# Kernel tuning notes

Measured on AMD Instinct MI355X. Metric: run time of the kernel, lower is better.

The kernel has to match this reference:

```python
import jax, jax.numpy as jnp
import numpy as np

T, B, IN, HID, OUT = 256, 64, 1024, 1024, 1024


def setup_inputs() -> dict:
    key = jax.random.key(0)
    ks = jax.random.split(key, 16)
    w = lambda k, i, o: (0.01 * jax.random.normal(k, (i, o), dtype=jnp.float32))
    return {
        "steps": jax.random.normal(ks[0], (T, B, IN), dtype=jnp.float32),
        "h": jax.random.normal(ks[1], (B, HID), dtype=jnp.float32),
        "c": jax.random.normal(ks[2], (B, HID), dtype=jnp.float32),
        "Wfx": w(ks[3], IN, HID), "Wfh": w(ks[4], HID, HID), "bf": jnp.zeros(HID, jnp.float32),
        "Wix": w(ks[5], IN, HID), "Wih": w(ks[6], HID, HID), "bi": jnp.zeros(HID, jnp.float32),
        "Wcx": w(ks[7], IN, HID), "Wch": w(ks[8], HID, HID), "bc": jnp.zeros(HID, jnp.float32),
        "Wox": w(ks[9], IN, HID), "Woh": w(ks[10], HID, HID), "bo": jnp.zeros(HID, jnp.float32),
        "Wy": w(ks[11], HID, OUT), "by": jnp.zeros(OUT, jnp.float32),
    }


def reference(steps, h, c, Wfx, Wfh, bf, Wix, Wih, bi, Wcx, Wch, bc,
              Wox, Woh, bo, Wy, by):
    def step(carry, x):
        h, c = carry
        F = jax.nn.sigmoid(x @ Wfx + h @ Wfh + bf)
        I = jax.nn.sigmoid(x @ Wix + h @ Wih + bi)
        cd = jnp.tanh(x @ Wcx + h @ Wch + bc)
        O = jax.nn.sigmoid(x @ Wox + h @ Woh + bo)
        c = F * c + I * cd
        h = jnp.tanh(c) * O
        y = h @ Wy + by  # [B, OUT]
        return (h, c), y

    (h, c), ys = jax.lax.scan(step, (h, c), steps)
    # torch.cat(outputs, dim=0) over T steps of [B, OUT] -> [T*B, OUT]
    return ys.reshape(-1, ys.shape[-1]), h, c
```

## Files before the change

### kernel.cpp

```cpp
#include <hip/hip_runtime.h>

typedef short short8 __attribute__((ext_vector_type(8)));
typedef float f32x4 __attribute__((ext_vector_type(4)));

__device__ __forceinline__ float bf2f(unsigned short s) {
    unsigned int u = ((unsigned int)s) << 16;
    return __builtin_bit_cast(float, u);
}
__device__ __forceinline__ unsigned short f2bf(float f) {
    unsigned int u = __builtin_bit_cast(unsigned int, f);
    u += 0x7fffu + ((u >> 16) & 1u);
    return (unsigned short)(u >> 16);
}
__device__ __forceinline__ float sigm(float x) { return 1.0f / (1.0f + __expf(-x)); }

__device__ __forceinline__ void gload16(const void* g, void* l) {
    __builtin_amdgcn_global_load_lds((const __attribute__((address_space(1))) void*)g,
                                     (__attribute__((address_space(3))) void*)l, 16, 0, 0);
}

__device__ __forceinline__ void at_swap64(unsigned long long* p, unsigned long long v) {
    asm volatile("global_atomic_swap_x2 %0, %1, off" :: "v"(p), "v"(v) : "memory");
}
__device__ __forceinline__ void at_add_nr(unsigned* p, unsigned v) {
    asm volatile("global_atomic_add %0, %1, off" :: "v"(p), "v"(v) : "memory");
}
__device__ __forceinline__ unsigned at_poll(unsigned* p) {
    unsigned v;
    asm volatile("global_atomic_add %0, %1, %2, off sc0\n\ts_waitcnt vmcnt(0)"
                 : "=v"(v) : "v"(p), "v"(0u) : "memory");
    return v;
}

#define WDOG_POLL 200000ull
#define WDOG_DEC  2000000ull
#define DEC_WAIT  10000ull

__global__ void conv_bf16(const float4* __restrict__ src, ushort4* __restrict__ dst, int n4) {
    for (int i = blockIdx.x * blockDim.x + threadIdx.x; i < n4; i += gridDim.x * blockDim.x) {
        float4 v = src[i];
        ushort4 o;
        o.x = f2bf(v.x); o.y = f2bf(v.y); o.z = f2bf(v.z); o.w = f2bf(v.w);
        dst[i] = o;
    }
}

struct PackArgs { const float* src[9]; };

__global__ __launch_bounds__(256) void pack_w(PackArgs pa,
                                              unsigned short* __restrict__ Wx,
                                              unsigned short* __restrict__ Wh,
                                              unsigned short* __restrict__ Wyt) {
    __shared__ float tile[32][33];
    const int z = blockIdx.z;
    const float* S = pa.src[z];
    unsigned short* D = (z < 4) ? Wx + (long)z * 1048576
                                : (z < 8) ? Wh + (long)(z - 4) * 1048576
                                          : Wyt;
    const int tx = threadIdx.x & 31, ty = threadIdx.x >> 5;
    const int rb = blockIdx.y * 32, cb = blockIdx.x * 32;
#pragma unroll
    for (int rr = 0; rr < 4; ++rr) {
        int r = ty + rr * 8;
        tile[r][tx] = S[(long)(rb + r) * 1024 + cb + tx];
    }
    __syncthreads();
#pragma unroll
    for (int rr = 0; rr < 4; ++rr) {
        int r = ty + rr * 8;
        D[(long)(cb + r) * 1024 + rb + tx] = f2bf(tile[tx][r]);
    }
}

__global__ void init_small(const float* __restrict__ h0,
                           const float* __restrict__ bf_, const float* __restrict__ bi_,
                           const float* __restrict__ bc_, const float* __restrict__ bo_,
                           unsigned short* __restrict__ hbuf0,
                           float* __restrict__ bcat, unsigned int* __restrict__ flags) {
    int i = blockIdx.x * blockDim.x + threadIdx.x;
    if (i < 1024) flags[i] = 0u;
    if (i < 65536) hbuf0[i] = f2bf(h0[i]);
    if (i < 4096) {
        const float* bs = (i < 1024) ? bf_ : (i < 2048) ? bi_ : (i < 3072) ? bc_ : bo_;
        bcat[i] = bs[i & 1023];
    }
}

template <int OUT_BF16>
__global__ __launch_bounds__(256) void gemm_bt(const unsigned short* __restrict__ A,
                                               const unsigned short* __restrict__ B,
                                               const float* __restrict__ bias,
                                               void* __restrict__ Cout,
                                               int M, int N, int K) {
    __shared__ unsigned short As[128 * 32];
    __shared__ unsigned short Bs[128 * 32];
    const int l = threadIdx.x;
    const int w = l >> 6, u = l & 63;
    const int wr = w >> 1, wc = w & 1;
    const long rowbase = (long)blockIdx.y * 128;
    const long colbase = (long)blockIdx.x * 128;

    f32x4 acc[4][4] = {};

    const int srow = l >> 2;
    const int sunit = l & 3;

    for (int k0 = 0; k0 < K; k0 += 32) {
#pragma unroll
        for (int i = 0; i < 2; ++i) {
            int row = i * 64 + srow;
            int su = sunit ^ (row & 3);
            gload16(&A[(rowbase + row) * K + k0 + su * 8], &As[i * 2048 + l * 8]);
            gload16(&B[(colbase + row) * K + k0 + su * 8], &Bs[i * 2048 + l * 8]);
        }
        __syncthreads();
        short8 a[4], b[4];
#pragma unroll
        for (int mi = 0; mi < 4; ++mi) {
            int row = wr * 64 + mi * 16 + (u & 15);
            a[mi] = *(const short8*)&As[row * 32 + (((u >> 4) ^ (row & 3))) * 8];
        }
#pragma unroll
        for (int ni = 0; ni < 4; ++ni) {
            int row = wc * 64 + ni * 16 + (u & 15);
            b[ni] = *(const short8*)&Bs[row * 32 + (((u >> 4) ^ (row & 3))) * 8];
        }
#pragma unroll
        for (int mi = 0; mi < 4; ++mi)
#pragma unroll
            for (int ni = 0; ni < 4; ++ni)
                acc[mi][ni] = __builtin_amdgcn_mfma_f32_16x16x32_bf16(a[mi], b[ni], acc[mi][ni], 0, 0, 0);
        __syncthreads();
    }

#pragma unroll
    for (int mi = 0; mi < 4; ++mi) {
#pragma unroll
        for (int ni = 0; ni < 4; ++ni) {
#pragma unroll
            for (int r = 0; r < 4; ++r) {
                long row = rowbase + wr * 64 + mi * 16 + (u >> 4) * 4 + r;
                long col = colbase + wc * 64 + ni * 16 + (u & 15);
                float v = acc[mi][ni][r] + bias[col];
                if (OUT_BF16)
                    ((unsigned short*)Cout)[row * N + col] = f2bf(v);
                else
                    ((float*)Cout)[row * N + col] = v;
            }
        }
    }
}

template <int FAST>
__device__ __forceinline__ void scan_go(
    int g, int i, int l, int w, int u,
    const unsigned short* __restrict__ Whc, const unsigned short* __restrict__ Xg,
    const unsigned short* __restrict__ h0bf, unsigned short* __restrict__ H,
    const float* __restrict__ c0, float* __restrict__ out_h, float* __restrict__ out_c,
    unsigned int* __restrict__ flags, f32x4 (*red)[8][64]) {

    const int rho = l >> 5, chi = l & 31;
    const int arow = u & 15;
    const int kofs = (u >> 4) * 8;

    short8 b[8][8];
#pragma unroll
    for (int n = 0; n < 8; ++n)
#pragma unroll
        for (int kt = 0; kt < 8; ++kt)
            b[n][kt] = *(const short8*)&Whc[(size_t)((n >> 1) * 1024 + 32 * i + 16 * (n & 1) + arow) * 1024
                                            + w * 256 + kt * 32 + kofs];

    float c = c0[(size_t)(8 * g + rho) * 1024 + 32 * i + chi];

    unsigned short xg[4];
#pragma unroll
    for (int ga = 0; ga < 4; ++ga)
        xg[ga] = Xg[(size_t)(8 * g + rho) * 4096 + ga * 1024 + 32 * i + chi];

    const short8 az = {};
    unsigned int* gctr = &flags[g * 16];

#pragma unroll 1
    for (int t = 0; t < 256; ++t) {
        const unsigned short* hp = t ? (H + (size_t)(t - 1) * 65536 + 8 * g * 1024)
                                     : (h0bf + 8 * g * 1024);
        const unsigned short* ab = hp + (size_t)arow * 1024 + w * 256 + kofs;

        f32x4 acc[8] = {};
#pragma unroll
        for (int kt = 0; kt < 8; ++kt) {
            short8 a = (arow < 8) ? *(const short8*)(ab + kt * 32) : az;
#pragma unroll
            for (int n = 0; n < 8; ++n)
                acc[n] = __builtin_amdgcn_mfma_f32_16x16x32_bf16(a, b[n][kt], acc[n], 0, 0, 0);
        }

#pragma unroll
        for (int n = 0; n < 8; ++n)
            red[w][n][u] = acc[n];
        __syncthreads();

        float pre[4];
#pragma unroll
        for (int ga = 0; ga < 4; ++ga) {
            int n = ga * 2 + (chi >> 4);
            int sl = ((rho >> 2) << 4) + (chi & 15);
            int rg = rho & 3;
            const float* r0 = (const float*)&red[0][n][sl];
            const float* r1 = (const float*)&red[1][n][sl];
            const float* r2 = (const float*)&red[2][n][sl];
            const float* r3 = (const float*)&red[3][n][sl];
            pre[ga] = r0[rg] + r1[rg] + r2[rg] + r3[rg] + bf2f(xg[ga]);
        }
        float F = sigm(pre[0]);
        float I = sigm(pre[1]);
        float Cd = tanhf(pre[2]);
        float O = sigm(pre[3]);
        float cn = F * c + I * Cd;
        c = cn;
        float hf = tanhf(cn) * O;

        const size_t hidx = (size_t)(t * 64 + 8 * g + rho) * 1024 + 32 * i + chi;
        if (FAST) {
            unsigned hv = (unsigned)f2bf(hf);
            unsigned p01 = hv | (__shfl_down(hv, 1) << 16);
            unsigned p23 = __shfl_down(p01, 2);
            if (!(chi & 3)) {
                unsigned long long v64 = (unsigned long long)p01 |
                                         ((unsigned long long)p23 << 32);
                at_swap64((unsigned long long*)&H[hidx], v64);
            }
        } else {
            __hip_atomic_store(&H[hidx], f2bf(hf), __ATOMIC_RELAXED, __HIP_MEMORY_SCOPE_AGENT);
        }
        if (t == 255) {
            out_h[(size_t)(8 * g + rho) * 1024 + 32 * i + chi] = hf;
            out_c[(size_t)(8 * g + rho) * 1024 + 32 * i + chi] = cn;
        }

        if (t < 255) {
            asm volatile("s_waitcnt vmcnt(0)" ::: "memory");
            __syncthreads();
            if (l == 0) {
                if (FAST)
                    at_add_nr(gctr, 1u);
                else
                    __hip_atomic_store(&flags[32 + g * 32 + i], (unsigned)(t + 1),
                                       __ATOMIC_RELAXED, __HIP_MEMORY_SCOPE_AGENT);
            }
#pragma unroll
            for (int ga = 0; ga < 4; ++ga)
                xg[ga] = Xg[(size_t)((t + 1) * 64 + 8 * g + rho) * 4096 + ga * 1024 + 32 * i + chi];

            if (FAST) {
                if (l == 0) {
                    const unsigned tgt = 32u * (unsigned)(t + 1);
                    unsigned long long wd0 = __builtin_amdgcn_s_memrealtime();
                    while (true) {
                        unsigned f = at_poll(gctr);
                        if (f >= tgt) break;
                        if (__builtin_amdgcn_s_memrealtime() - wd0 > WDOG_POLL) break;
                        __builtin_amdgcn_s_sleep(4);
                    }
                }
                __syncthreads();
            } else {
                const unsigned tgt = (unsigned)(t + 1);
                unsigned long long wd0 = __builtin_amdgcn_s_memrealtime();
                while (true) {
                    unsigned f = (u < 8) ? __hip_atomic_load(&flags[32 + g * 32 + 8 * w + u],
                                                             __ATOMIC_RELAXED, __HIP_MEMORY_SCOPE_AGENT)
                                         : tgt;
                    if (__all(f >= tgt)) break;
                    if (__builtin_amdgcn_s_memrealtime() - wd0 > WDOG_POLL) break;
                    __builtin_amdgcn_s_sleep(2);
                }
            }
            asm volatile("" ::: "memory");
            __builtin_amdgcn_sched_barrier(0);
        }
    }
}

__device__ __forceinline__ void scan64(
    int bid, int l, int w, int u,
    const unsigned short* __restrict__ Whc, const unsigned short* __restrict__ Xg,
    const unsigned short* __restrict__ h0bf, unsigned short* __restrict__ H,
    const float* __restrict__ c0, float* __restrict__ out_h, float* __restrict__ out_c,
    unsigned int* __restrict__ flags, f32x4 (*red)[4][4][64], unsigned short* hs) {

    const int j0 = bid * 16;
    const int jj = u & 15, q = u >> 4;

    short8 b[4][8];
#pragma unroll
    for (int g = 0; g < 4; ++g)
#pragma unroll
        for (int kt = 0; kt < 8; ++kt)
            b[g][kt] = *(const short8*)&Whc[(size_t)(g * 1024 + j0 + jj) * 1024 + w * 256 + kt * 32 + q * 8];

    float c[4];
#pragma unroll
    for (int r = 0; r < 4; ++r)
        c[r] = c0[(size_t)(w * 16 + q * 4 + r) * 1024 + j0 + jj];

    unsigned short xg[4][4];
#pragma unroll
    for (int g = 0; g < 4; ++g)
#pragma unroll
        for (int r = 0; r < 4; ++r)
            xg[g][r] = Xg[(size_t)(w * 16 + q * 4 + r) * 4096 + g * 1024 + j0 + jj];

    const int srow_ = l >> 2, sqtr = l & 3;

#pragma unroll 1
    for (int t = 0; t < 256; ++t) {
        const unsigned short* hp = t ? (H + (size_t)(t - 1) * 65536) : h0bf;

        f32x4 acc[4][4] = {};
#pragma unroll
        for (int kt = 0; kt < 8; ++kt) {
            short8 a[4];
#pragma unroll
            for (int m = 0; m < 4; ++m)
                a[m] = *(const short8*)&hp[(size_t)(m * 16 + jj) * 1024 + w * 256 + kt * 32 + q * 8];
#pragma unroll
            for (int m = 0; m < 4; ++m)
#pragma unroll
                for (int g = 0; g < 4; ++g)
                    acc[m][g] = __builtin_amdgcn_mfma_f32_16x16x32_bf16(a[m], b[g][kt], acc[m][g], 0, 0, 0);
        }

        __syncthreads();
#pragma unroll
        for (int m = 0; m < 4; ++m)
#pragma unroll
            for (int g = 0; g < 4; ++g)
                red[m][w][g][u] = acc[m][g];
        __syncthreads();
        f32x4 gate[4];
#pragma unroll
        for (int g = 0; g < 4; ++g) {
            gate[g] = red[w][0][g][u];
#pragma unroll
            for (int w2 = 1; w2 < 4; ++w2)
                gate[g] += red[w][w2][g][u];
        }

#pragma unroll
        for (int r = 0; r < 4; ++r) {
            float F = sigm(gate[0][r] + bf2f(xg[0][r]));
            float I = sigm(gate[1][r] + bf2f(xg[1][r]));
            float Cd = tanhf(gate[2][r] + bf2f(xg[2][r]));
            float O = sigm(gate[3][r] + bf2f(xg[3][r]));
            float cn = F * c[r] + I * Cd;
            c[r] = cn;
            float hf = tanhf(cn) * O;
            int row = w * 16 + q * 4 + r;
            hs[row * 16 + jj] = f2bf(hf);
            if (t == 255) {
                out_h[(size_t)row * 1024 + j0 + jj] = hf;
                out_c[(size_t)row * 1024 + j0 + jj] = cn;
            }
        }
        __syncthreads();

        {
            unsigned long long v = *(const unsigned long long*)&hs[srow_ * 16 + sqtr * 4];
            __hip_atomic_store((unsigned long long*)&H[(size_t)(t * 64 + srow_) * 1024 + j0 + sqtr * 4],
                               v, __ATOMIC_RELAXED, __HIP_MEMORY_SCOPE_AGENT);
        }

        if (t < 255) {
            asm volatile("s_waitcnt vmcnt(0)" ::: "memory");
            __syncthreads();
            if (l == 0)
                __hip_atomic_store(&flags[512 + bid], (unsigned)(t + 1),
                                   __ATOMIC_RELAXED, __HIP_MEMORY_SCOPE_AGENT);
#pragma unroll
            for (int g = 0; g < 4; ++g)
#pragma unroll
                for (int r = 0; r < 4; ++r)
                    xg[g][r] = Xg[(size_t)((t + 1) * 64 + w * 16 + q * 4 + r) * 4096 + g * 1024 + j0 + jj];
            const unsigned tgt = (unsigned)(t + 1);
            unsigned long long wd0 = __builtin_amdgcn_s_memrealtime();
            while (true) {
                unsigned f = __hip_atomic_load(&flags[512 + 16 * w + jj], __ATOMIC_RELAXED,
                                               __HIP_MEMORY_SCOPE_AGENT);
                if (__all(f >= tgt)) break;
                if (__builtin_amdgcn_s_memrealtime() - wd0 > WDOG_POLL) break;
                __builtin_amdgcn_s_sleep(4);
            }
            asm volatile("" ::: "memory");
            __builtin_amdgcn_sched_barrier(0);
        }
    }
}

__global__ __launch_bounds__(256, 1) void lstm_scan(
    const unsigned short* __restrict__ Whc, const unsigned short* __restrict__ Xg,
    const unsigned short* __restrict__ h0bf, unsigned short* __restrict__ H,
    const float* __restrict__ c0, float* __restrict__ out_h, float* __restrict__ out_c,
    unsigned int* __restrict__ flags) {
    __shared__ __align__(16) char smem_[67584];
    __shared__ int s_dec;
    __shared__ int s_allsame;
    const int l = threadIdx.x, w = l >> 6, u = l & 63;
    const int bid = blockIdx.x;

    if (l == 0) {
        __hip_atomic_fetch_add(&flags[576], 1u, __ATOMIC_RELAXED, __HIP_MEMORY_SCOPE_AGENT);
        unsigned dec = 0;
        if (bid == 0) {
            unsigned long long t0 = __builtin_amdgcn_s_memrealtime();
            while (true) {
                unsigned cnt = __hip_atomic_load(&flags[576], __ATOMIC_RELAXED,
                                                 __HIP_MEMORY_SCOPE_AGENT);
                if (cnt >= 256u) { dec = 1u; break; }
                if (__builtin_amdgcn_s_memrealtime() - t0 > DEC_WAIT) { dec = 2u; break; }
                __builtin_amdgcn_s_sleep(8);
            }
            __hip_atomic_store(&flags[577], dec, __ATOMIC_RELAXED, __HIP_MEMORY_SCOPE_AGENT);
        } else {
            unsigned long long t0 = __builtin_amdgcn_s_memrealtime();
            while (true) {
                dec = __hip_atomic_load(&flags[577], __ATOMIC_RELAXED, __HIP_MEMORY_SCOPE_AGENT);
                if (dec) break;
                if (__builtin_amdgcn_s_memrealtime() - t0 > WDOG_DEC) { dec = 2u; break; }
                __builtin_amdgcn_s_sleep(8);
            }
        }
        s_dec = (int)dec;
    }
    __syncthreads();

    if (s_dec == 1) {
        const int g = bid & 7, i = bid >> 3;
        unsigned int* xcc = flags + 256;
        unsigned my_xcc;
        asm volatile("s_getreg_b32 %0, hwreg(HW_REG_XCC_ID)" : "=s"(my_xcc));
        if (l == 0)
            __hip_atomic_store(&xcc[bid], 256u | (my_xcc & 255u),
                               __ATOMIC_RELAXED, __HIP_MEMORY_SCOPE_AGENT);
        if (w == 0) {
            unsigned v = 256u;
            unsigned long long wd0 = __builtin_amdgcn_s_memrealtime();
            int timeout = 0;
            while (true) {
                v = (u < 32) ? __hip_atomic_load(&xcc[(u << 3) | g], __ATOMIC_RELAXED,
                                                 __HIP_MEMORY_SCOPE_AGENT)
                             : 257u;
                unsigned long long rdy = __ballot(v >= 256u);
                if (rdy == ~0ull) break;
                if (__builtin_amdgcn_s_memrealtime() - wd0 > WDOG_DEC) { timeout = 1; break; }
                __builtin_amdgcn_s_sleep(8);
            }
            unsigned first = __shfl(v, 0);
            int same = ((u < 32) ? (v == first) : 1) ? 1 : 0;
            unsigned long long m = __ballot(same);
            if (u == 0) s_allsame = (!timeout && m == ~0ull) ? 1 : 0;
        }
        __syncthreads();

        f32x4 (*red)[8][64] = (f32x4(*)[8][64])smem_;
        if (s_allsame)
            scan_go<1>(g, i, l, w, u, Whc, Xg, h0bf, H, c0, out_h, out_c, flags, red);
        else
            scan_go<0>(g, i, l, w, u, Whc, Xg, h0bf, H, c0, out_h, out_c, flags, red);
    } else {
        if (bid >= 64) return;
        f32x4 (*red64)[4][4][64] = (f32x4(*)[4][4][64])smem_;
        unsigned short* hs = (unsigned short*)(smem_ + 65536);
        scan64(bid, l, w, u, Whc, Xg, h0bf, H, c0, out_h, out_c, flags, red64, hs);
    }
}

extern "C" void kernel_launch(void* const* d_in, const int* in_sizes, int n_in,
                              void* d_out, int out_size, void* d_ws, size_t ws_size,
                              hipStream_t stream) {
    const float* steps = (const float*)d_in[0];
    const float* h0 = (const float*)d_in[1];
    const float* c0 = (const float*)d_in[2];
    const float* Wfx = (const float*)d_in[3];
    const float* Wfh = (const float*)d_in[4];
    const float* bf_ = (const float*)d_in[5];
    const float* Wix = (const float*)d_in[6];
    const float* Wih = (const float*)d_in[7];
    const float* bi_ = (const float*)d_in[8];
    const float* Wcx = (const float*)d_in[9];
    const float* Wch = (const float*)d_in[10];
    const float* bc_ = (const float*)d_in[11];
    const float* Wox = (const float*)d_in[12];
    const float* Woh = (const float*)d_in[13];
    const float* bo_ = (const float*)d_in[14];
    const float* Wy = (const float*)d_in[15];
    const float* by_ = (const float*)d_in[16];

    char* ws = (char*)d_ws;
    unsigned short* Xbf = (unsigned short*)(ws + 0L);
    unsigned short* Xg  = (unsigned short*)(ws + 33554432L);
    unsigned short* H   = (unsigned short*)(ws + 167772160L);
    unsigned short* Wx  = (unsigned short*)(ws + 201326592L);
    unsigned short* Wh  = (unsigned short*)(ws + 209715200L);
    unsigned short* Wyt = (unsigned short*)(ws + 218103808L);
    float* bcat         = (float*)(ws + 220200960L);
    unsigned short* hbuf0 = (unsigned short*)(ws + 220217344L);
    unsigned int* flags = (unsigned int*)(ws + 220348416L);

    float* out_y = (float*)d_out;
    float* out_h = out_y + 16777216L;
    float* out_c = out_h + 65536L;

    conv_bf16<<<2048, 256, 0, stream>>>((const float4*)steps, (ushort4*)Xbf, 4194304);

    PackArgs pa;
    pa.src[0] = Wfx; pa.src[1] = Wix; pa.src[2] = Wcx; pa.src[3] = Wox;
    pa.src[4] = Wfh; pa.src[5] = Wih; pa.src[6] = Wch; pa.src[7] = Woh;
    pa.src[8] = Wy;
    pack_w<<<dim3(32, 32, 9), 256, 0, stream>>>(pa, Wx, Wh, Wyt);

    init_small<<<256, 256, 0, stream>>>(h0, bf_, bi_, bc_, bo_, hbuf0, bcat, flags);

    gemm_bt<1><<<dim3(32, 128), 256, 0, stream>>>(Xbf, Wx, bcat, Xg, 16384, 4096, 1024);

    lstm_scan<<<256, 256, 0, stream>>>(Wh, Xg, hbuf0, H, c0, out_h, out_c, flags);

    gemm_bt<0><<<dim3(8, 128), 256, 0, stream>>>(H, Wyt, by_, (void*)d_out, 16384, 1024, 1024);
}
```

Measured before the change: 1.402 ms.

## Double scan block size to 512 threads, splitting MFMA gate columns across waves

The recurrent scan kernel now launches 512 threads per block. In the fast path, the eight waves split the gate-column tiles in two halves, so each wave holds half as many weight fragments and issues half as many MFMAs per step. The epilogue stays on the first 256 threads. The slow fallback path leaves the extra waves idle. Flag offsets move to new slots, and the thread-0 load of the next x-gates is deferred until after the spin wait. The aim is to shorten the per-step serial matmul latency, at the cost of more barrier participants and register pressure under a 512-thread launch bound.

```diff
diff --git a/kernel.cpp b/kernel.cpp
--- a/kernel.cpp
+++ b/kernel.cpp
@@ -35,6 +35,7 @@
 #define WDOG_POLL 200000ull
 #define WDOG_DEC  2000000ull
 #define DEC_WAIT  10000ull
+
 
 __global__ void conv_bf16(const float4* __restrict__ src, ushort4* __restrict__ dst, int n4) {
     for (int i = blockIdx.x * blockDim.x + threadIdx.x; i < n4; i += gridDim.x * blockDim.x) {
@@ -159,84 +160,90 @@
     const float* __restrict__ c0, float* __restrict__ out_h, float* __restrict__ out_c,
     unsigned int* __restrict__ flags, f32x4 (*red)[8][64]) {
 
-    const int rho = l >> 5, chi = l & 31;
+    const int s = w & 3, nh = w >> 2;
+    const int rho = (l & 255) >> 5, chi = l & 31;
     const int arow = u & 15;
     const int kofs = (u >> 4) * 8;
-
-    short8 b[8][8];
-#pragma unroll
-    for (int n = 0; n < 8; ++n)
+    const int epi = (l < 256);
+
+    short8 b[4][8];
+#pragma unroll
+    for (int ga = 0; ga < 4; ++ga)
 #pragma unroll
         for (int kt = 0; kt < 8; ++kt)
-            b[n][kt] = *(const short8*)&Whc[(size_t)((n >> 1) * 1024 + 32 * i + 16 * (n & 1) + arow) * 1024
-                                            + w * 256 + kt * 32 + kofs];
-
-    float c = c0[(size_t)(8 * g + rho) * 1024 + 32 * i + chi];
-
-    unsigned short xg[4];
-#pragma unroll
-    for (int ga = 0; ga < 4; ++ga)
-        xg[ga] = Xg[(size_t)(8 * g + rho) * 4096 + ga * 1024 + 32 * i + chi];
+            b[ga][kt] = *(const short8*)&Whc[(size_t)(ga * 1024 + 32 * i + 16 * nh + arow) * 1024
+                                             + s * 256 + kt * 32 + kofs];
+
+    float c = 0.f;
+    unsigned short xg[4] = {};
+    if (epi) {
+        c = c0[(size_t)(8 * g + rho) * 1024 + 32 * i + chi];
+#pragma unroll
+        for (int ga = 0; ga < 4; ++ga)
+            xg[ga] = Xg[(size_t)(8 * g + rho) * 4096 + ga * 1024 + 32 * i + chi];
+    }
 
     const short8 az = {};
-    unsigned int* gctr = &flags[g * 16];
+    unsigned int* gctr = &flags[640 + g * 16];
 
 #pragma unroll 1
     for (int t = 0; t < 256; ++t) {
         const unsigned short* hp = t ? (H + (size_t)(t - 1) * 65536 + 8 * g * 1024)
                                      : (h0bf + 8 * g * 1024);
-        const unsigned short* ab = hp + (size_t)arow * 1024 + w * 256 + kofs;
-
-        f32x4 acc[8] = {};
+        const unsigned short* ab = hp + (size_t)arow * 1024 + s * 256 + kofs;
+
+        f32x4 acc[4] = {};
 #pragma unroll
         for (int kt = 0; kt < 8; ++kt) {
             short8 a = (arow < 8) ? *(const short8*)(ab + kt * 32) : az;
 #pragma unroll
-            for (int n = 0; n < 8; ++n)
-                acc[n] = __builtin_amdgcn_mfma_f32_16x16x32_bf16(a, b[n][kt], acc[n], 0, 0, 0);
-        }
-
-#pragma unroll
-        for (int n = 0; n < 8; ++n)
-            red[w][n][u] = acc[n];
-        __syncthreads();
-
-        float pre[4];
-#pragma unroll
-        for (int ga = 0; ga < 4; ++ga) {
-            int n = ga * 2 + (chi >> 4);
-            int sl = ((rho >> 2) << 4) + (chi & 15);
-            int rg = rho & 3;
-            const float* r0 = (const float*)&red[0][n][sl];
-            const float* r1 = (const float*)&red[1][n][sl];
-            const float* r2 = (const float*)&red[2][n][sl];
-            const float* r3 = (const float*)&red[3][n][sl];
-            pre[ga] = r0[rg] + r1[rg] + r2[rg] + r3[rg] + bf2f(xg[ga]);
-        }
-        float F = sigm(pre[0]);
-        float I = sigm(pre[1]);
-        float Cd = tanhf(pre[2]);
-        float O = sigm(pre[3]);
-        float cn = F * c + I * Cd;
-        c = cn;
-        float hf = tanhf(cn) * O;
-
-        const size_t hidx = (size_t)(t * 64 + 8 * g + rho) * 1024 + 32 * i + chi;
-        if (FAST) {
-            unsigned hv = (unsigned)f2bf(hf);
-            unsigned p01 = hv | (__shfl_down(hv, 1) << 16);
-            unsigned p23 = __shfl_down(p01, 2);
-            if (!(chi & 3)) {
-                unsigned long long v64 = (unsigned long long)p01 |
-                                         ((unsigned long long)p23 << 32);
-                at_swap64((unsigned long long*)&H[hidx], v64);
-            }
-        } else {
-            __hip_atomic_store(&H[hidx], f2bf(hf), __ATOMIC_RELAXED, __HIP_MEMORY_SCOPE_AGENT);
-        }
-        if (t == 255) {
-            out_h[(size_t)(8 * g + rho) * 1024 + 32 * i + chi] = hf;
-            out_c[(size_t)(8 * g + rho) * 1024 + 32 * i + chi] = cn;
+            for (int ga = 0; ga < 4; ++ga)
+                acc[ga] = __builtin_amdgcn_mfma_f32_16x16x32_bf16(a, b[ga][kt], acc[ga], 0, 0, 0);
+        }
+
+#pragma unroll
+        for (int ga = 0; ga < 4; ++ga)
+            red[s][ga * 2 + nh][u] = acc[ga];
+        __syncthreads();
+
+        if (epi) {
+            float pre[4];
+#pragma unroll
+            for (int ga = 0; ga < 4; ++ga) {
+                int n = ga * 2 + (chi >> 4);
+                int sl = ((rho >> 2) << 4) + (chi & 15);
+                int rg = rho & 3;
+                const float* r0 = (const float*)&red[0][n][sl];
+                const float* r1 = (const float*)&red[1][n][sl];
+                const float* r2 = (const float*)&red[2][n][sl];
+                const float* r3 = (const float*)&red[3][n][sl];
+                pre[ga] = r0[rg] + r1[rg] + r2[rg] + r3[rg] + bf2f(xg[ga]);
+            }
+            float F = sigm(pre[0]);
+            float I = sigm(pre[1]);
+            float Cd = tanhf(pre[2]);
+            float O = sigm(pre[3]);
+            float cn = F * c + I * Cd;
+            c = cn;
+            float hf = tanhf(cn) * O;
+
+            const size_t hidx = (size_t)(t * 64 + 8 * g + rho) * 1024 + 32 * i + chi;
+            if (FAST) {
+                unsigned hv = (unsigned)f2bf(hf);
+                unsigned p01 = hv | (__shfl_down(hv, 1) << 16);
+                unsigned p23 = __shfl_down(p01, 2);
+                if (!(chi & 3)) {
+                    unsigned long long v64 = (unsigned long long)p01 |
+                                             ((unsigned long long)p23 << 32);
+                    at_swap64((unsigned long long*)&H[hidx], v64);
+                }
+            } else {
+                __hip_atomic_store(&H[hidx], f2bf(hf), __ATOMIC_RELAXED, __HIP_MEMORY_SCOPE_AGENT);
+            }
+            if (t == 255) {
+                out_h[(size_t)(8 * g + rho) * 1024 + 32 * i + chi] = hf;
+                out_c[(size_t)(8 * g + rho) * 1024 + 32 * i + chi] = cn;
+            }
         }
 
         if (t < 255) {
@@ -246,13 +253,14 @@
                 if (FAST)
                     at_add_nr(gctr, 1u);
                 else
-                    __hip_atomic_store(&flags[32 + g * 32 + i], (unsigned)(t + 1),
+                    __hip_atomic_store(&flags[768 + g * 32 + i], (unsigned)(t + 1),
                                        __ATOMIC_RELAXED, __HIP_MEMORY_SCOPE_AGENT);
             }
-#pragma unroll
-            for (int ga = 0; ga < 4; ++ga)
-                xg[ga] = Xg[(size_t)((t + 1) * 64 + 8 * g + rho) * 4096 + ga * 1024 + 32 * i + chi];
-
+            if (epi && l > 0) {
+#pragma unroll
+                for (int ga = 0; ga < 4; ++ga)
+                    xg[ga] = Xg[(size_t)((t + 1) * 64 + 8 * g + rho) * 4096 + ga * 1024 + 32 * i + chi];
+            }
             if (FAST) {
                 if (l == 0) {
                     const unsigned tgt = 32u * (unsigned)(t + 1);
@@ -265,17 +273,23 @@
                     }
                 }
                 __syncthreads();
+                if (l == 0) {
+#pragma unroll
+                    for (int ga = 0; ga < 4; ++ga)
+                        xg[ga] = Xg[(size_t)((t + 1) * 64 + 8 * g + rho) * 4096 + ga * 1024 + 32 * i + chi];
+                }
             } else {
                 const unsigned tgt = (unsigned)(t + 1);
                 unsigned long long wd0 = __builtin_amdgcn_s_memrealtime();
                 while (true) {
-                    unsigned f = (u < 8) ? __hip_atomic_load(&flags[32 + g * 32 + 8 * w + u],
+                    unsigned f = (u < 8) ? __hip_atomic_load(&flags[768 + g * 32 + 8 * s + u],
                                                              __ATOMIC_RELAXED, __HIP_MEMORY_SCOPE_AGENT)
                                          : tgt;
                     if (__all(f >= tgt)) break;
                     if (__builtin_amdgcn_s_memrealtime() - wd0 > WDOG_POLL) break;
                     __builtin_amdgcn_s_sleep(2);
                 }
+                __syncthreads();
             }
             asm volatile("" ::: "memory");
             __builtin_amdgcn_sched_barrier(0);
@@ -292,81 +306,88 @@
 
     const int j0 = bid * 16;
     const int jj = u & 15, q = u >> 4;
-
-    short8 b[4][8];
-#pragma unroll
-    for (int g = 0; g < 4; ++g)
-#pragma unroll
-        for (int kt = 0; kt < 8; ++kt)
-            b[g][kt] = *(const short8*)&Whc[(size_t)(g * 1024 + j0 + jj) * 1024 + w * 256 + kt * 32 + q * 8];
-
-    float c[4];
-#pragma unroll
-    for (int r = 0; r < 4; ++r)
-        c[r] = c0[(size_t)(w * 16 + q * 4 + r) * 1024 + j0 + jj];
-
-    unsigned short xg[4][4];
-#pragma unroll
-    for (int g = 0; g < 4; ++g)
+    const int act = (w < 4);
+
+    short8 b[4][8] = {};
+    float c[4] = {};
+    unsigned short xg[4][4] = {};
+    if (act) {
+#pragma unroll
+        for (int g = 0; g < 4; ++g)
+#pragma unroll
+            for (int kt = 0; kt < 8; ++kt)
+                b[g][kt] = *(const short8*)&Whc[(size_t)(g * 1024 + j0 + jj) * 1024 + w * 256 + kt * 32 + q * 8];
 #pragma unroll
         for (int r = 0; r < 4; ++r)
-            xg[g][r] = Xg[(size_t)(w * 16 + q * 4 + r) * 4096 + g * 1024 + j0 + jj];
-
-    const int srow_ = l >> 2, sqtr = l & 3;
+            c[r] = c0[(size_t)(w * 16 + q * 4 + r) * 1024 + j0 + jj];
+#pragma unroll
+        for (int g = 0; g < 4; ++g)
+#pragma unroll
+            for (int r = 0; r < 4; ++r)
+                xg[g][r] = Xg[(size_t)(w * 16 + q * 4 + r) * 4096 + g * 1024 + j0 + jj];
+    }
+
+    const int srow_ = (l & 255) >> 2, sqtr = l & 3;
 
 #pragma unroll 1
     for (int t = 0; t < 256; ++t) {
         const unsigned short* hp = t ? (H + (size_t)(t - 1) * 65536) : h0bf;
 
         f32x4 acc[4][4] = {};
-#pragma unroll
-        for (int kt = 0; kt < 8; ++kt) {
-            short8 a[4];
+        if (act) {
+#pragma unroll
+            for (int kt = 0; kt < 8; ++kt) {
+                short8 a[4];
+#pragma unroll
+                for (int m = 0; m < 4; ++m)
+                    a[m] = *(const short8*)&hp[(size_t)(m * 16 + jj) * 1024 + w * 256 + kt * 32 + q * 8];
+#pragma unroll
+                for (int m = 0; m < 4; ++m)
+#pragma unroll
+                    for (int g = 0; g < 4; ++g)
+                        acc[m][g] = __builtin_amdgcn_mfma_f32_16x16x32_bf16(a[m], b[g][kt], acc[m][g], 0, 0, 0);
+            }
+        }
+
+        __syncthreads();
+        if (act) {
 #pragma unroll
             for (int m = 0; m < 4; ++m)
-                a[m] = *(const short8*)&hp[(size_t)(m * 16 + jj) * 1024 + w * 256 + kt * 32 + q * 8];
-#pragma unroll
-            for (int m = 0; m < 4; ++m)
 #pragma unroll
                 for (int g = 0; g < 4; ++g)
-                    acc[m][g] = __builtin_amdgcn_mfma_f32_16x16x32_bf16(a[m], b[g][kt], acc[m][g], 0, 0, 0);
-        }
-
-        __syncthreads();
-#pragma unroll
-        for (int m = 0; m < 4; ++m)
-#pragma unroll
-            for (int g = 0; g < 4; ++g)
-                red[m][w][g][u] = acc[m][g];
-        __syncthreads();
-        f32x4 gate[4];
-#pragma unroll
-        for (int g = 0; g < 4; ++g) {
-            gate[g] = red[w][0][g][u];
-#pragma unroll
-            for (int w2 = 1; w2 < 4; ++w2)
-                gate[g] += red[w][w2][g][u];
-        }
-
-#pragma unroll
-        for (int r = 0; r < 4; ++r) {
-            float F = sigm(gate[0][r] + bf2f(xg[0][r]));
-            float I = sigm(gate[1][r] + bf2f(xg[1][r]));
-            float Cd = tanhf(gate[2][r] + bf2f(xg[2][r]));
-            float O = sigm(gate[3][r] + bf2f(xg[3][r]));
-            float cn = F * c[r] + I * Cd;
-            c[r] = cn;
-            float hf = tanhf(cn) * O;
-            int row = w * 16 + q * 4 + r;
-            hs[row * 16 + jj] = f2bf(hf);
-            if (t == 255) {
-                out_h[(size_t)row * 1024 + j0 + jj] = hf;
-                out_c[(size_t)row * 1024 + j0 + jj] = cn;
-            }
-        }
-        __syncthreads();
-
-        {
+                    red[m][w][g][u] = acc[m][g];
+        }
+        __syncthreads();
+
+        if (act) {
+            f32x4 gate[4];
+#pragma unroll
+            for (int g = 0; g < 4; ++g) {
+                gate[g] = red[w][0][g][u];
+#pragma unroll
+                for (int w2 = 1; w2 < 4; ++w2)
+                    gate[g] += red[w][w2][g][u];
+            }
+#pragma unroll
+            for (int r = 0; r < 4; ++r) {
+                float F = sigm(gate[0][r] + bf2f(xg[0][r]));
+                float I = sigm(gate[1][r] + bf2f(xg[1][r]));
+                float Cd = tanhf(gate[2][r] + bf2f(xg[2][r]));
+                float O = sigm(gate[3][r] + bf2f(xg[3][r]));
+                float cn = F * c[r] + I * Cd;
+                c[r] = cn;
+                float hf = tanhf(cn) * O;
+                int row = w * 16 + q * 4 + r;
+                hs[row * 16 + jj] = f2bf(hf);
+                if (t == 255) {
+                    out_h[(size_t)row * 1024 + j0 + jj] = hf;
+                    out_c[(size_t)row * 1024 + j0 + jj] = cn;
+                }
+            }
+        }
+        __syncthreads();
+
+        if (l < 256) {
             unsigned long long v = *(const unsigned long long*)&hs[srow_ * 16 + sqtr * 4];
             __hip_atomic_store((unsigned long long*)&H[(size_t)(t * 64 + srow_) * 1024 + j0 + sqtr * 4],
                                v, __ATOMIC_RELAXED, __HIP_MEMORY_SCOPE_AGENT);
@@ -378,16 +399,19 @@
             if (l == 0)
                 __hip_atomic_store(&flags[512 + bid], (unsigned)(t + 1),
                                    __ATOMIC_RELAXED, __HIP_MEMORY_SCOPE_AGENT);
-#pragma unroll
-            for (int g = 0; g < 4; ++g)
-#pragma unroll
-                for (int r = 0; r < 4; ++r)
-                    xg[g][r] = Xg[(size_t)((t + 1) * 64 + w * 16 + q * 4 + r) * 4096 + g * 1024 + j0 + jj];
+            if (act) {
+#pragma unroll
+                for (int g = 0; g < 4; ++g)
+#pragma unroll
+                    for (int r = 0; r < 4; ++r)
+                        xg[g][r] = Xg[(size_t)((t + 1) * 64 + w * 16 + q * 4 + r) * 4096 + g * 1024 + j0 + jj];
+            }
             const unsigned tgt = (unsigned)(t + 1);
             unsigned long long wd0 = __builtin_amdgcn_s_memrealtime();
             while (true) {
-                unsigned f = __hip_atomic_load(&flags[512 + 16 * w + jj], __ATOMIC_RELAXED,
-                                               __HIP_MEMORY_SCOPE_AGENT);
+                unsigned f = (act && jj < 16) ? __hip_atomic_load(&flags[512 + 16 * w + jj],
+                                                                  __ATOMIC_RELAXED, __HIP_MEMORY_SCOPE_AGENT)
+                                              : tgt;
                 if (__all(f >= tgt)) break;
                 if (__builtin_amdgcn_s_memrealtime() - wd0 > WDOG_POLL) break;
                 __builtin_amdgcn_s_sleep(4);
@@ -398,7 +422,7 @@
     }
 }
 
-__global__ __launch_bounds__(256, 1) void lstm_scan(
+__global__ __launch_bounds__(512, 1) void lstm_scan(
     const unsigned short* __restrict__ Whc, const unsigned short* __restrict__ Xg,
     const unsigned short* __restrict__ h0bf, unsigned short* __restrict__ H,
     const float* __restrict__ c0, float* __restrict__ out_h, float* __restrict__ out_c,
@@ -524,7 +548,7 @@
 
     gemm_bt<1><<<dim3(32, 128), 256, 0, stream>>>(Xbf, Wx, bcat, Xg, 16384, 4096, 1024);
 
-    lstm_scan<<<256, 256, 0, stream>>>(Wh, Xg, hbuf0, H, c0, out_h, out_c, flags);
+    lstm_scan<<<256, 512, 0, stream>>>(Wh, Xg, hbuf0, H, c0, out_h, out_c, flags);
 
     gemm_bt<0><<<dim3(8, 128), 256, 0, stream>>>(H, Wyt, by_, (void*)d_out, 16384, 1024, 1024);
 }
```

After: 1.311 ms. 6.6% less time.
